# Kernel tuning notes

Measured on AMD Instinct MI355X. Metric: run time of the kernel, lower is better.

## Reference

```python
import math
import jax, jax.numpy as jnp
import numpy as np

B, T, E, H = 1, 2048, 2048, 16
D = E // H // 2  # head_dim = 64
DEPTH = 12
LAMBDA_INIT = 0.8 - 0.6 * math.exp(-0.3 * DEPTH)
EPS = 1e-5
NEG = -1e30


def rotary_cos_sin(seqlen, dim):
    # matches flash-attn RotaryEmbedding: inv_freq over even indices, base 10000
    inv_freq = 1.0 / (10000.0 ** (jnp.arange(0, dim, 2, dtype=jnp.float32) / dim))
    t = jnp.arange(seqlen, dtype=jnp.float32)
    freqs = jnp.outer(t, inv_freq)  # [T, D/2]
    return jnp.cos(freqs), jnp.sin(freqs)


def apply_rotary_interleaved(x, cos, sin):
    # x: [B, T, nH, D]; rotate interleaved pairs (x0,x1),(x2,x3),...
    x1 = x[..., 0::2]
    x2 = x[..., 1::2]
    c = cos[None, :, None, :]
    s = sin[None, :, None, :]
    o1 = x1 * c - x2 * s
    o2 = x1 * s + x2 * c
    return jnp.stack([o1, o2], axis=-1).reshape(x.shape)


def causal_attn_pair(q, k, v1, v2, mask, scale):
    # q,k,v*: [B, T, H, D]; shared softmax over (q,k), applied to both v1 and v2
    s = jnp.einsum('bthd,bshd->bhts', q, k) * scale
    s = jnp.where(mask, s, NEG)
    a = jax.nn.softmax(s, axis=-1)
    o1 = jnp.einsum('bhts,bshd->bthd', a, v1)
    o2 = jnp.einsum('bhts,bshd->bthd', a, v2)
    return jnp.concatenate([o1, o2], axis=-1)  # [B, T, H, 2D]


def setup_inputs() -> dict:
    key = jax.random.key(0)
    ks = jax.random.split(key, 10)
    return {
        'query': jax.random.normal(ks[0], (B, T, E), dtype=jnp.float32),
        'Wq': jax.random.normal(ks[1], (E, E), dtype=jnp.float32) * 0.02,
        'Wk': jax.random.normal(ks[2], (E, E), dtype=jnp.float32) * 0.02,
        'Wv': jax.random.normal(ks[3], (E, E), dtype=jnp.float32) * 0.02,
        'Wout': jax.random.normal(ks[4], (E, E), dtype=jnp.float32) * 0.02,
        'lambda_q1': jax.random.normal(ks[5], (D,), dtype=jnp.float32) * 0.1,
        'lambda_k1': jax.random.normal(ks[6], (D,), dtype=jnp.float32) * 0.1,
        'lambda_q2': jax.random.normal(ks[7], (D,), dtype=jnp.float32) * 0.1,
        'lambda_k2': jax.random.normal(ks[8], (D,), dtype=jnp.float32) * 0.1,
        'rms_weight': jnp.ones((2 * D,), dtype=jnp.float32),
    }


def reference(query, Wq, Wk, Wv, Wout, lambda_q1, lambda_k1, lambda_q2, lambda_k2, rms_weight):
    bsz, tgt_len, embed_dim = query.shape
    cos, sin = rotary_cos_sin(tgt_len, D)
    scale = D ** (-0.5)
    mask = jnp.tril(jnp.ones((tgt_len, tgt_len), dtype=bool))[None, None]

    q = (query @ Wq).reshape(bsz, tgt_len, 2 * H, D)
    k = (query @ Wk).reshape(bsz, tgt_len, 2 * H, D)
    v = (query @ Wv).reshape(bsz, tgt_len, H, 2, D)

    q = apply_rotary_emb = apply_rotary_interleaved(q, cos, sin)
    k = apply_rotary_interleaved(k, cos, sin)

    q = q.reshape(bsz, tgt_len, H, 2, D)
    k = k.reshape(bsz, tgt_len, H, 2, D)
    q1, q2 = q[:, :, :, 0], q[:, :, :, 1]
    k1, k2 = k[:, :, :, 0], k[:, :, :, 1]
    v1, v2 = v[:, :, :, 0], v[:, :, :, 1]

    attn1 = causal_attn_pair(q1, k1, v1, v2, mask, scale)  # [B,T,H,2D]
    attn2 = causal_attn_pair(q2, k2, v1, v2, mask, scale)

    lambda_1 = jnp.exp(jnp.sum(lambda_q1 * lambda_k1))
    lambda_2 = jnp.exp(jnp.sum(lambda_q2 * lambda_k2))
    lambda_full = lambda_1 - lambda_2 + LAMBDA_INIT

    f1 = jnp.fft.rfft(attn1, axis=1)
    f2 = jnp.fft.rfft(attn2, axis=1)
    attn_freq = f1 - lambda_full * f2

    n_freq = attn_freq.shape[1]
    sigma = 0.3 / 2.0  # cutoff_ratio / 2, gaussian window
    x = jnp.linspace(0.0, 1.0, n_freq)
    filt = jnp.exp(-0.5 * (x / sigma) ** 2)
    attn_freq = attn_freq * filt[None, :, None, None]

    attn = jnp.fft.irfft(attn_freq, n=tgt_len, axis=1)  # [B,T,H,2D]

    # RMSNorm over last dim (2*head_dim) with affine weight
    attn = attn * jax.lax.rsqrt(jnp.mean(attn * attn, axis=-1, keepdims=True) + EPS) * rms_weight
    attn = attn * (1.0 - LAMBDA_INIT)

    attn = attn.reshape(bsz, tgt_len, H * 2 * D)
    return attn @ Wout
```

## Files before the change

kernel.cpp:

```cpp
#include <hip/hip_runtime.h>
#include <math.h>

#define LAMBDA_INIT_F 0.7836057665316245f
#define ONE_MINUS_LI  0.2163942334683755f

typedef unsigned short ushort_t;
typedef unsigned int   uint32;
typedef unsigned long long u64;
typedef __attribute__((ext_vector_type(8))) short short8;
typedef __attribute__((ext_vector_type(4))) float f32x4;

__device__ __forceinline__ ushort_t f2bf(float f) {
    union { float f; uint32 u; } x; x.f = f;
    uint32 r = (x.u + 0x7fffu + ((x.u >> 16) & 1u)) >> 16;
    return (ushort_t)r;
}

__device__ __forceinline__ void gld16(ushort_t* lds, const ushort_t* g) {
    __builtin_amdgcn_global_load_lds(
        (const __attribute__((address_space(1))) uint32*)g,
        (__attribute__((address_space(3))) uint32*)lds,
        16, 0, 0);
}

__global__ __launch_bounds__(64) void lambda_kernel(
    const float* __restrict__ lq1, const float* __restrict__ lk1,
    const float* __restrict__ lq2, const float* __restrict__ lk2,
    float* __restrict__ lam)
{
    int l = threadIdx.x;
    float p1 = lq1[l] * lk1[l];
    float p2 = lq2[l] * lk2[l];
    for (int off = 32; off; off >>= 1) {
        p1 += __shfl_down(p1, off);
        p2 += __shfl_down(p2, off);
    }
    if (l == 0) lam[0] = expf(p1) - expf(p2) + LAMBDA_INIT_F;
}

__global__ __launch_bounds__(256) void gfilt_kernel(float* __restrict__ g)
{
    __shared__ float red[4];
    const int j = blockIdx.x;
    int tau = j - 64;
    int ta = tau < 0 ? -tau : tau;
    const int tid = threadIdx.x;
    float acc = 0.0f;
    for (int k = tid; k <= 1024; k += 256) {
        float w = (k == 0 || k == 1024) ? 1.0f : 2.0f;
        float r = (float)k * (1.0f / 153.6f);
        float f = expf(-0.5f * r * r);
        int m = (k * ta) & 2047;
        float ang = (float)m * 3.0679615757712823e-3f;
        acc += w * f * cosf(ang);
    }
    for (int off = 32; off; off >>= 1) acc += __shfl_down(acc, off);
    if ((tid & 63) == 0) red[tid >> 6] = acc;
    __syncthreads();
    if (tid == 0)
        g[j] = (red[0] + red[1] + red[2] + red[3]) * (1.0f / 2048.0f);
}

__global__ __launch_bounds__(256) void rottab(float* __restrict__ ct, float* __restrict__ st)
{
    int id = blockIdx.x * 256 + threadIdx.x;
    int t = id >> 5, i = id & 31;
    double inv = exp(-0.28782313662425575 * (double)i);
    double a = (double)t * inv;
    ct[id] = (float)cos(a);
    st[id] = (float)sin(a);
}

__global__ __launch_bounds__(256) void cvt_bf16(const float* __restrict__ s, ushort_t* __restrict__ d)
{
    int i = (blockIdx.x * 256 + threadIdx.x) * 8;
    float4 a = *(const float4*)(s + i);
    float4 b = *(const float4*)(s + i + 4);
    uint4 pk;
    pk.x = (uint32)f2bf(a.x) | ((uint32)f2bf(a.y) << 16);
    pk.y = (uint32)f2bf(a.z) | ((uint32)f2bf(a.w) << 16);
    pk.z = (uint32)f2bf(b.x) | ((uint32)f2bf(b.y) << 16);
    pk.w = (uint32)f2bf(b.z) | ((uint32)f2bf(b.w) << 16);
    *(uint4*)(d + i) = pk;
}

__global__ __launch_bounds__(256) void wtrans(
    const float* __restrict__ Wq, const float* __restrict__ Wk,
    const float* __restrict__ Wv, const float* __restrict__ Wo,
    ushort_t* __restrict__ Tq, ushort_t* __restrict__ Tk,
    ushort_t* __restrict__ Tv, ushort_t* __restrict__ To)
{
    int z = blockIdx.z;
    const float* S = (z == 0) ? Wq : (z == 1) ? Wk : (z == 2) ? Wv : Wo;
    ushort_t* Dt = (z == 0) ? Tq : (z == 1) ? Tk : (z == 2) ? Tv : To;
    bool perm = (z < 2);
    __shared__ float Ls[64 * 65];
    const int tid = threadIdx.x;
    const int n0 = blockIdx.x * 64, k0 = blockIdx.y * 64;
    #pragma unroll
    for (int it = 0; it < 4; ++it) {
        int kk = it * 16 + (tid >> 4);
        int nn = (tid & 15) * 4;
        float4 v = *(const float4*)(S + (size_t)(k0 + kk) * 2048 + n0 + nn);
        Ls[(nn + 0) * 65 + kk] = v.x;
        Ls[(nn + 1) * 65 + kk] = v.y;
        Ls[(nn + 2) * 65 + kk] = v.z;
        Ls[(nn + 3) * 65 + kk] = v.w;
    }
    __syncthreads();
    int nl = tid >> 2, kc = (tid & 3) * 16;
    int ng = n0 + nl;
    int nd = perm ? ((ng & ~63) | ((ng & 1) << 5) | ((ng & 63) >> 1)) : ng;
    uint4 p0, p1;
    const float* row = Ls + nl * 65 + kc;
    p0.x = (uint32)f2bf(row[0])  | ((uint32)f2bf(row[1])  << 16);
    p0.y = (uint32)f2bf(row[2])  | ((uint32)f2bf(row[3])  << 16);
    p0.z = (uint32)f2bf(row[4])  | ((uint32)f2bf(row[5])  << 16);
    p0.w = (uint32)f2bf(row[6])  | ((uint32)f2bf(row[7])  << 16);
    p1.x = (uint32)f2bf(row[8])  | ((uint32)f2bf(row[9])  << 16);
    p1.y = (uint32)f2bf(row[10]) | ((uint32)f2bf(row[11]) << 16);
    p1.z = (uint32)f2bf(row[12]) | ((uint32)f2bf(row[13]) << 16);
    p1.w = (uint32)f2bf(row[14]) | ((uint32)f2bf(row[15]) << 16);
    *(uint4*)(Dt + (size_t)nd * 2048 + k0 + kc) = p0;
    *(uint4*)(Dt + (size_t)nd * 2048 + k0 + kc + 8) = p1;
}

template<int QA, int QB, bool RA>
__device__ __forceinline__ void qkv_phase(
    const ushort_t* __restrict__ Ah, const ushort_t* __restrict__ Bh,
    short8 af[8], f32x4 acc[8][4], int wr, int wc, int quad, int l15)
{
    if (RA) {
        #pragma unroll
        for (int m = 0; m < 4; ++m)
            #pragma unroll
            for (int ks = 0; ks < 2; ++ks) {
                int r = wr * 64 + m * 16 + l15;
                af[m * 2 + ks] = *(const short8*)(Ah + r * 64 + ((ks * 4 + quad) ^ (r & 7)) * 8);
            }
    }
    short8 bfr[4];
    #pragma unroll
    for (int n = 0; n < 2; ++n)
        #pragma unroll
        for (int ks = 0; ks < 2; ++ks) {
            int r = (wc >> 1) * 64 + (wc & 1) * 16 + n * 32 + l15;
            bfr[n * 2 + ks] = *(const short8*)(Bh + r * 64 + ((ks * 4 + quad) ^ (r & 7)) * 8);
        }
    __builtin_amdgcn_s_setprio(1);
    #pragma unroll
    for (int m = 0; m < 4; ++m)
        #pragma unroll
        for (int n = 0; n < 2; ++n)
            #pragma unroll
            for (int ks = 0; ks < 2; ++ks)
                acc[QA * 4 + m][QB * 2 + n] = __builtin_amdgcn_mfma_f32_16x16x32_bf16(
                    af[m * 2 + ks], bfr[n * 2 + ks], acc[QA * 4 + m][QB * 2 + n], 0, 0, 0);
    __builtin_amdgcn_s_setprio(0);
}

#define PH_SYNC() do { __builtin_amdgcn_s_barrier(); __builtin_amdgcn_sched_barrier(0); } while (0)

__global__ __launch_bounds__(512, 2) void gemm_qkv(
    const ushort_t* __restrict__ A, const ushort_t* __restrict__ WT,
    ushort_t* __restrict__ q1, ushort_t* __restrict__ q2,
    ushort_t* __restrict__ k1, ushort_t* __restrict__ k2,
    ushort_t* __restrict__ v1T, ushort_t* __restrict__ v2T,
    const float* __restrict__ ctab, const float* __restrict__ stab)
{
    __shared__ ushort_t As[2][2][8192];
    __shared__ ushort_t Bs[2][2][8192];
    const int tid = threadIdx.x;
    const int w = tid >> 6, lane = tid & 63;
    const int quad = lane >> 4, l15 = lane & 15;
    const int wr = w >> 2, wc = w & 3;
    const int rb = blockIdx.y * 256, cbg = blockIdx.x * 256;

    auto stageA = [&](int pr, int ha, int tau) {
        int k0 = tau * 64;
        #pragma unroll
        for (int u = 0; u < 2; ++u) {
            int ci = w * 128 + u * 64 + lane;
            int row = ci >> 3, cc = (ci & 7) ^ (row & 7);
            gld16(&As[pr][ha][(w * 128 + u * 64) * 8],
                  A + (size_t)(rb + ha * 128 + row) * 2048 + k0 + cc * 8);
        }
    };
    auto stageB = [&](int pr, int hb, int tau) {
        int k0 = tau * 64;
        #pragma unroll
        for (int u = 0; u < 2; ++u) {
            int ci = w * 128 + u * 64 + lane;
            int row = ci >> 3, cc = (ci & 7) ^ (row & 7);
            gld16(&Bs[pr][hb][(w * 128 + u * 64) * 8],
                  WT + (size_t)(cbg + hb * 128 + row) * 2048 + k0 + cc * 8);
        }
    };

    stageA(0, 0, 0); stageB(0, 0, 0);
    stageA(0, 1, 0); stageB(0, 1, 0);
    stageA(1, 0, 1); stageB(1, 0, 1);

    f32x4 acc[8][4];
    #pragma unroll
    for (int i = 0; i < 8; ++i)
        #pragma unroll
        for (int j = 0; j < 4; ++j) acc[i][j] = (f32x4)0.0f;
    short8 af[8];

    for (int it = 0; it < 16; ++it) {
        const int t = it * 2;
        const int t2 = (t + 2 < 32) ? t + 2 : 31;
        const int t3 = (t + 3 < 32) ? t + 3 : 31;
        asm volatile("s_waitcnt vmcnt(8)" ::: "memory");
        PH_SYNC();
        stageA(1, 1, t + 1);
        qkv_phase<0, 0, true >(As[0][0], Bs[0][0], af, acc, wr, wc, quad, l15);
        asm volatile("s_waitcnt vmcnt(6)" ::: "memory");
        PH_SYNC();
        stageB(1, 1, t + 1);
        qkv_phase<0, 1, false>(As[0][0], Bs[0][1], af, acc, wr, wc, quad, l15);
        PH_SYNC();
        stageA(0, 0, t2);
        qkv_phase<1, 0, true >(As[0][1], Bs[0][0], af, acc, wr, wc, quad, l15);
        PH_SYNC();
        stageB(0, 0, t2);
        qkv_phase<1, 1, false>(As[0][1], Bs[0][1], af, acc, wr, wc, quad, l15);
        asm volatile("s_waitcnt vmcnt(8)" ::: "memory");
        PH_SYNC();
        stageA(0, 1, t2);
        qkv_phase<0, 0, true >(As[1][0], Bs[1][0], af, acc, wr, wc, quad, l15);
        asm volatile("s_waitcnt vmcnt(6)" ::: "memory");
        PH_SYNC();
        stageB(0, 1, t2);
        qkv_phase<0, 1, false>(As[1][0], Bs[1][1], af, acc, wr, wc, quad, l15);
        PH_SYNC();
        stageA(1, 0, t3);
        qkv_phase<1, 0, true >(As[1][1], Bs[1][0], af, acc, wr, wc, quad, l15);
        PH_SYNC();
        stageB(1, 0, t3);
        qkv_phase<1, 1, false>(As[1][1], Bs[1][1], af, acc, wr, wc, quad, l15);
    }

    const int region = cbg >> 11;
    const int nloc = cbg & 2047;
    if (region < 2) {
        ushort_t* b1 = region ? k1 : q1;
        ushort_t* b2 = region ? k2 : q2;
        const int i = (wc & 1) * 16 + l15;
        #pragma unroll
        for (int qb = 0; qb < 2; ++qb) {
            int head2 = (nloc >> 6) + qb * 2 + (wc >> 1);
            ushort_t* dst = ((head2 & 1) ? b2 : b1) + (size_t)(head2 >> 1) * 2048 * 64;
            #pragma unroll
            for (int mi = 0; mi < 8; ++mi)
                #pragma unroll
                for (int r = 0; r < 4; ++r) {
                    int t = rb + (mi >> 2) * 128 + wr * 64 + (mi & 3) * 16 + quad * 4 + r;
                    float c = ctab[t * 32 + i], s = stab[t * 32 + i];
                    float x1 = acc[mi][qb * 2 + 0][r], x2 = acc[mi][qb * 2 + 1][r];
                    dst[(size_t)t * 64 + i]      = f2bf(x1 * c - x2 * s);
                    dst[(size_t)t * 64 + 32 + i] = f2bf(x1 * s + x2 * c);
                }
        }
    } else {
        #pragma unroll
        for (int mi = 0; mi < 8; ++mi)
            #pragma unroll
            for (int nj = 0; nj < 4; ++nj) {
                int cg = nloc + (nj >> 1) * 128 + (wc >> 1) * 64 + (wc & 1) * 16
                       + (nj & 1) * 32 + l15;
                int hh = cg >> 7, pr = (cg >> 6) & 1, d = cg & 63;
                int tb = rb + (mi >> 2) * 128 + wr * 64 + (mi & 3) * 16 + quad * 4;
                ushort_t* dst = (pr ? v2T : v1T) + ((size_t)(hh * 64 + d)) * 2048 + tb;
                u64 pk = (u64)f2bf(acc[mi][nj][0])
                       | ((u64)f2bf(acc[mi][nj][1]) << 16)
                       | ((u64)f2bf(acc[mi][nj][2]) << 32)
                       | ((u64)f2bf(acc[mi][nj][3]) << 48);
                *(u64*)dst = pk;
            }
    }
}

#define PSTRIDE 88

__device__ __forceinline__ void attn_step(
    const ushort_t* __restrict__ Kb, const ushort_t* __restrict__ V1b,
    const ushort_t* __restrict__ V2b, ushort_t* __restrict__ pw,
    const short8* qb, f32x4* O, float& m_i, float& l_i,
    int quad, int l15, int row_l, bool diag)
{
    f32x4 s[4];
    #pragma unroll
    for (int j = 0; j < 4; ++j) s[j] = (f32x4)0.0f;
    #pragma unroll
    for (int ks = 0; ks < 2; ++ks)
        #pragma unroll
        for (int j = 0; j < 4; ++j) {
            int r = j * 16 + l15;
            short8 kf = *(const short8*)(Kb + r * 64 + ((ks * 4 + quad) ^ (r & 7)) * 8);
            s[j] = __builtin_amdgcn_mfma_f32_16x16x32_bf16(kf, qb[ks], s[j], 0, 0, 0);
        }
    float mx = -1e30f;
    #pragma unroll
    for (int j = 0; j < 4; ++j)
        #pragma unroll
        for (int r = 0; r < 4; ++r) {
            float v = s[j][r] * 0.125f;
            if (diag) {
                int kp = j * 16 + quad * 4 + r;
                v = (kp <= row_l) ? v : -1e30f;
            }
            s[j][r] = v;
            mx = fmaxf(mx, v);
        }
    mx = fmaxf(mx, __shfl_xor(mx, 16));
    mx = fmaxf(mx, __shfl_xor(mx, 32));
    float newm = fmaxf(m_i, mx);
    float alpha = __expf(m_i - newm);
    float sum = 0.0f;
    #pragma unroll
    for (int j = 0; j < 4; ++j) {
        float p0 = __expf(s[j][0] - newm);
        float p1 = __expf(s[j][1] - newm);
        float p2 = __expf(s[j][2] - newm);
        float p3 = __expf(s[j][3] - newm);
        sum += (p0 + p1) + (p2 + p3);
        u64 pk = (u64)f2bf(p0) | ((u64)f2bf(p1) << 16)
               | ((u64)f2bf(p2) << 32) | ((u64)f2bf(p3) << 48);
        *(u64*)(pw + l15 * PSTRIDE + j * 16 + quad * 4) = pk;
    }
    sum += __shfl_xor(sum, 16);
    sum += __shfl_xor(sum, 32);
    l_i = l_i * alpha + sum;
    m_i = newm;
    float av0 = __shfl(alpha, quad * 4 + 0);
    float av1 = __shfl(alpha, quad * 4 + 1);
    float av2 = __shfl(alpha, quad * 4 + 2);
    float av3 = __shfl(alpha, quad * 4 + 3);
    #pragma unroll
    for (int nt = 0; nt < 8; ++nt) {
        O[nt][0] *= av0; O[nt][1] *= av1; O[nt][2] *= av2; O[nt][3] *= av3;
    }
    #pragma unroll
    for (int ks = 0; ks < 2; ++ks) {
        short8 pf = *(const short8*)(pw + l15 * PSTRIDE + ks * 32 + quad * 8);
        #pragma unroll
        for (int nt = 0; nt < 8; ++nt) {
            const ushort_t* Vs = (nt < 4) ? V1b : V2b;
            int d = (nt & 3) * 16 + l15;
            short8 vf = *(const short8*)(Vs + d * 64 + ((ks * 4 + quad) ^ (d & 7)) * 8);
            O[nt] = __builtin_amdgcn_mfma_f32_16x16x32_bf16(pf, vf, O[nt], 0, 0, 0);
        }
    }
}

__global__ __launch_bounds__(512, 4) void attn_pipe(
    const ushort_t* __restrict__ q1, const ushort_t* __restrict__ k1,
    const ushort_t* __restrict__ q2, const ushort_t* __restrict__ k2,
    const ushort_t* __restrict__ v1T, const ushort_t* __restrict__ v2T,
    float* __restrict__ X, const float* __restrict__ lam_ptr)
{
    __shared__ ushort_t Tt[4][4096];
    __shared__ ushort_t Ps[8][16 * PSTRIDE];

    const int tid = threadIdx.x;
    const int w = tid >> 6, lane = tid & 63;
    const int quad = lane >> 4, l15 = lane & 15;
    const int pair = w >> 2, wl = w & 3;
    const int b = blockIdx.x;
    const int h = b & 15;
    const int x16 = (b & 255) >> 4;
    const int qt = (b < 256) ? (31 - x16) : x16;
    const float lam = lam_ptr[0];
    const int row_l = wl * 16 + l15;

    const ushort_t* k1h = k1 + (size_t)h * 2048 * 64;
    const ushort_t* k2h = k2 + (size_t)h * 2048 * 64;
    const ushort_t* v1h = v1T + (size_t)h * 64 * 2048;
    const ushort_t* v2h = v2T + (size_t)h * 64 * 2048;

    short8 qb[2];
    {
        const ushort_t* qp = (pair ? q2 : q1)
            + ((size_t)h * 2048 + qt * 64 + wl * 16 + l15) * 64 + quad * 8;
        qb[0] = *(const short8*)(qp);
        qb[1] = *(const short8*)(qp + 32);
    }

    const int ci = tid;
    const int srow = ci >> 3, scc = (ci & 7) ^ (srow & 7);
    const int koff = srow * 64 + scc * 8;
    const int voff = srow * 2048 + scc * 8;

    short8 sK1, sK2, sV1, sV2;

    sK1 = *(const short8*)(k1h + koff);
    sK2 = *(const short8*)(k2h + koff);
    sV1 = *(const short8*)(v1h + voff);
    sV2 = *(const short8*)(v2h + voff);
    *(short8*)(&Tt[0][ci * 8]) = sK1;
    *(short8*)(&Tt[1][ci * 8]) = sK2;
    *(short8*)(&Tt[2][ci * 8]) = sV1;
    *(short8*)(&Tt[3][ci * 8]) = sV2;
    __syncthreads();

    f32x4 O[8];
    #pragma unroll
    for (int i = 0; i < 8; ++i) O[i] = (f32x4)0.0f;
    float m_i = -1e30f, l_i = 0.0f;

    const ushort_t* Kb = Tt[pair];

    for (int kt = 0; kt <= qt; ++kt) {
        if (kt < qt) {
            int kb = (kt + 1) * 4096, vb = (kt + 1) * 64;
            sK1 = *(const short8*)(k1h + kb + koff);
            sK2 = *(const short8*)(k2h + kb + koff);
            sV1 = *(const short8*)(v1h + vb + voff);
            sV2 = *(const short8*)(v2h + vb + voff);
        }
        attn_step(Kb, Tt[2], Tt[3], &Ps[w][0], qb, O, m_i, l_i,
                  quad, l15, row_l, kt == qt);
        __syncthreads();
        if (kt < qt) {
            *(short8*)(&Tt[0][ci * 8]) = sK1;
            *(short8*)(&Tt[1][ci * 8]) = sK2;
            *(short8*)(&Tt[2][ci * 8]) = sV1;
            *(short8*)(&Tt[3][ci * 8]) = sV2;
            __syncthreads();
        }
    }

    float sc = pair ? lam : 1.0f;
    float rr0 = sc / __shfl(l_i, quad * 4 + 0);
    float rr1 = sc / __shfl(l_i, quad * 4 + 1);
    float rr2 = sc / __shfl(l_i, quad * 4 + 2);
    float rr3 = sc / __shfl(l_i, quad * 4 + 3);

    float* LX = (float*)&Tt[0][0];
    const int rbase = wl * 16 + quad * 4;
    if (pair) {
        #pragma unroll
        for (int nt = 0; nt < 8; ++nt) {
            int cb = nt * 16 + l15;
            LX[(rbase + 0) * 128 + cb] = O[nt][0] * rr0;
            LX[(rbase + 1) * 128 + cb] = O[nt][1] * rr1;
            LX[(rbase + 2) * 128 + cb] = O[nt][2] * rr2;
            LX[(rbase + 3) * 128 + cb] = O[nt][3] * rr3;
        }
    }
    __syncthreads();
    if (!pair) {
        int tb = qt * 64 + rbase;
        #pragma unroll
        for (int nt = 0; nt < 8; ++nt) {
            int cb = nt * 16 + l15;
            int col = h * 128 + cb;
            X[(size_t)(tb + 0) * 2048 + col] = O[nt][0] * rr0 - LX[(rbase + 0) * 128 + cb];
            X[(size_t)(tb + 1) * 2048 + col] = O[nt][1] * rr1 - LX[(rbase + 1) * 128 + cb];
            X[(size_t)(tb + 2) * 2048 + col] = O[nt][2] * rr2 - LX[(rbase + 2) * 128 + cb];
            X[(size_t)(tb + 3) * 2048 + col] = O[nt][3] * rr3 - LX[(rbase + 3) * 128 + cb];
        }
    }
}

__global__ __launch_bounds__(256) void conv_t(
    const float* __restrict__ X, const float* __restrict__ g, float* __restrict__ Y)
{
    __shared__ float Xs[192 * 64];
    __shared__ float gs[129];
    const int tid = threadIdx.x;
    const int c0 = blockIdx.x * 64, t0 = blockIdx.y * 64;
    const int c = tid & 63, tg = tid >> 6;
    for (int j = tg; j < 192; j += 4)
        Xs[j * 64 + c] = X[(size_t)((t0 - 64 + j) & 2047) * 2048 + c0 + c];
    if (tid < 129) gs[tid] = g[tid];
    __syncthreads();
    float accv[16];
    #pragma unroll
    for (int i = 0; i < 16; ++i) accv[i] = 0.0f;
    const int tl0 = tg * 16;
    for (int tap = 0; tap < 129; ++tap) {
        float gv = gs[tap];
        int base = (tl0 + 128 - tap) * 64 + c;
        #pragma unroll
        for (int i = 0; i < 16; ++i) accv[i] += gv * Xs[base + i * 64];
    }
    #pragma unroll
    for (int i = 0; i < 16; ++i)
        Y[(size_t)(t0 + tl0 + i) * 2048 + c0 + c] = accv[i];
}

__global__ __launch_bounds__(64) void rms_bf(
    const float* __restrict__ Y, const float* __restrict__ wgt, ushort_t* __restrict__ yb)
{
    int grp = blockIdx.x;
    int t = grp >> 4, hh = grp & 15, l = threadIdx.x;
    size_t base = (size_t)t * 2048 + hh * 128;
    float a = Y[base + l];
    float b = Y[base + 64 + l];
    float ss = a * a + b * b;
    for (int off = 32; off; off >>= 1) ss += __shfl_down(ss, off);
    ss = __shfl(ss, 0);
    float r = rsqrtf(ss * (1.0f / 128.0f) + 1e-5f) * ONE_MINUS_LI;
    yb[base + l]      = f2bf(a * r * wgt[l]);
    yb[base + 64 + l] = f2bf(b * r * wgt[64 + l]);
}

__global__ __launch_bounds__(256) void gemm_out(
    const ushort_t* __restrict__ A, const ushort_t* __restrict__ BT,
    float* __restrict__ C)
{
    __shared__ ushort_t As[4096];
    __shared__ ushort_t Bs[8192];
    const int tid = threadIdx.x;
    const int w = tid >> 6, lane = tid & 63;
    const int quad = lane >> 4, l15 = lane & 15;
    const int wr = w >> 1, wc = w & 1;
    const int rb = blockIdx.y * 64, cb = blockIdx.x * 128;

    f32x4 acc[2][4];
    #pragma unroll
    for (int i = 0; i < 2; ++i)
        #pragma unroll
        for (int j = 0; j < 4; ++j) acc[i][j] = (f32x4)0.0f;

    for (int k0 = 0; k0 < 2048; k0 += 64) {
        #pragma unroll
        for (int u = 0; u < 2; ++u) {
            int off = (w * 2 + u) * 512;
            int Lc = (off >> 3) + lane;
            int row = Lc >> 3, cc = (Lc & 7) ^ (row & 7);
            gld16(As + off, A + (size_t)(rb + row) * 2048 + k0 + cc * 8);
        }
        #pragma unroll
        for (int u = 0; u < 4; ++u) {
            int off = (w * 4 + u) * 512;
            int Lc = (off >> 3) + lane;
            int row = Lc >> 3, cc = (Lc & 7) ^ (row & 7);
            gld16(Bs + off, BT + (size_t)(cb + row) * 2048 + k0 + cc * 8);
        }
        __syncthreads();
        #pragma unroll
        for (int ks = 0; ks < 2; ++ks) {
            short8 af[2], bfr[4];
            #pragma unroll
            for (int mi = 0; mi < 2; ++mi) {
                int r = wr * 32 + mi * 16 + l15;
                af[mi] = *(const short8*)(As + r * 64 + ((ks * 4 + quad) ^ (r & 7)) * 8);
            }
            #pragma unroll
            for (int nj = 0; nj < 4; ++nj) {
                int r = wc * 64 + nj * 16 + l15;
                bfr[nj] = *(const short8*)(Bs + r * 64 + ((ks * 4 + quad) ^ (r & 7)) * 8);
            }
            #pragma unroll
            for (int mi = 0; mi < 2; ++mi)
                #pragma unroll
                for (int nj = 0; nj < 4; ++nj)
                    acc[mi][nj] = __builtin_amdgcn_mfma_f32_16x16x32_bf16(
                        af[mi], bfr[nj], acc[mi][nj], 0, 0, 0);
        }
        __syncthreads();
    }

    #pragma unroll
    for (int mi = 0; mi < 2; ++mi)
        #pragma unroll
        for (int nj = 0; nj < 4; ++nj) {
            int cg = cb + wc * 64 + nj * 16 + l15;
            #pragma unroll
            for (int r = 0; r < 4; ++r) {
                int t = rb + wr * 32 + mi * 16 + quad * 4 + r;
                C[(size_t)t * 2048 + cg] = acc[mi][nj][r];
            }
        }
}

extern "C" void kernel_launch(void* const* d_in, const int* in_sizes, int n_in,
                              void* d_out, int out_size, void* d_ws, size_t ws_size,
                              hipStream_t stream)
{
    const float* query = (const float*)d_in[0];
    const float* Wq    = (const float*)d_in[1];
    const float* Wk    = (const float*)d_in[2];
    const float* Wv    = (const float*)d_in[3];
    const float* Wout  = (const float*)d_in[4];
    const float* lq1   = (const float*)d_in[5];
    const float* lk1   = (const float*)d_in[6];
    const float* lq2   = (const float*)d_in[7];
    const float* lk2   = (const float*)d_in[8];
    const float* rmsw  = (const float*)d_in[9];
    float* out = (float*)d_out;

    const size_t MB = 1ull << 20;
    char* W = (char*)d_ws;
    ushort_t* WqT   = (ushort_t*)(W + 0 * MB);
    ushort_t* WkT   = (ushort_t*)(W + 8 * MB);
    ushort_t* WvT   = (ushort_t*)(W + 16 * MB);
    ushort_t* WoutT = (ushort_t*)(W + 24 * MB);
    ushort_t* qb    = (ushort_t*)(W + 32 * MB);
    ushort_t* q1    = (ushort_t*)(W + 40 * MB);
    ushort_t* q2    = (ushort_t*)(W + 44 * MB);
    ushort_t* k1    = (ushort_t*)(W + 48 * MB);
    ushort_t* k2    = (ushort_t*)(W + 52 * MB);
    ushort_t* v1T   = (ushort_t*)(W + 56 * MB);
    ushort_t* v2T   = (ushort_t*)(W + 60 * MB);
    float*    X     = (float*)   (W + 64 * MB);
    float*    Y     = (float*)   (W + 32 * MB);
    ushort_t* ybf   = (ushort_t*)(W + 48 * MB);
    float*    ctab  = (float*)   (W + 80 * MB);
    float*    stab  = (float*)   (W + 80 * MB + 256 * 1024);
    float*    gbuf  = (float*)   (W + 80 * MB + 512 * 1024);
    float*    lam   = (float*)   (W + 80 * MB + 520 * 1024);

    lambda_kernel<<<1, 64, 0, stream>>>(lq1, lk1, lq2, lk2, lam);
    gfilt_kernel<<<129, 256, 0, stream>>>(gbuf);
    rottab<<<256, 256, 0, stream>>>(ctab, stab);
    cvt_bf16<<<2048, 256, 0, stream>>>(query, qb);
    wtrans<<<dim3(32, 32, 4), 256, 0, stream>>>(Wq, Wk, Wv, Wout, WqT, WkT, WvT, WoutT);

    gemm_qkv<<<dim3(24, 8), 512, 0, stream>>>(qb, WqT, q1, q2, k1, k2, v1T, v2T, ctab, stab);

    attn_pipe<<<512, 512, 0, stream>>>(q1, k1, q2, k2, v1T, v2T, X, lam);

    conv_t<<<dim3(32, 32), 256, 0, stream>>>(X, gbuf, Y);
    rms_bf<<<32768, 64, 0, stream>>>(Y, rmsw, ybf);

    gemm_out<<<dim3(16, 32), 256, 0, stream>>>(ybf, WoutT, out);
}
```

Measured before the change: 337.8 us.

## Restructure QKV GEMM main loop into ping-pong phases with explicit LDS waits

The QKV projection GEMM loop is rescheduled so each phase issues its LDS fragment reads and the next global-to-LDS prefetch first, then synchronizes with barriers and an explicit lgkmcnt(0) wait before the MFMA block. The vmcnt waits are moved and the staging order changes, with separate named LDS buffers in place of the indexed array. The aim is to overlap LDS reads and global prefetch with MFMA work across waves and to give the scheduler clearer phase boundaries. The added barriers per phase and the changed prefetch order could add sync overhead or expose races if the wait counts are off.

```diff
diff --git a/kernel.cpp b/kernel.cpp
--- a/kernel.cpp
+++ b/kernel.cpp
@@ -125,28 +125,33 @@
     *(uint4*)(Dt + (size_t)nd * 2048 + k0 + kc + 8) = p1;
 }
 
-template<int QA, int QB, bool RA>
-__device__ __forceinline__ void qkv_phase(
-    const ushort_t* __restrict__ Ah, const ushort_t* __restrict__ Bh,
-    short8 af[8], f32x4 acc[8][4], int wr, int wc, int quad, int l15)
-{
-    if (RA) {
-        #pragma unroll
-        for (int m = 0; m < 4; ++m)
-            #pragma unroll
-            for (int ks = 0; ks < 2; ++ks) {
-                int r = wr * 64 + m * 16 + l15;
-                af[m * 2 + ks] = *(const short8*)(Ah + r * 64 + ((ks * 4 + quad) ^ (r & 7)) * 8);
-            }
-    }
-    short8 bfr[4];
-    #pragma unroll
-    for (int n = 0; n < 2; ++n)
-        #pragma unroll
-        for (int ks = 0; ks < 2; ++ks) {
-            int r = (wc >> 1) * 64 + (wc & 1) * 16 + n * 32 + l15;
-            bfr[n * 2 + ks] = *(const short8*)(Bh + r * 64 + ((ks * 4 + quad) ^ (r & 7)) * 8);
-        }
+#define SB()    __builtin_amdgcn_s_barrier()
+#define LGKM0() asm volatile("s_waitcnt lgkmcnt(0)" ::: "memory")
+#define VM6()   asm volatile("s_waitcnt vmcnt(6)" ::: "memory")
+
+__device__ __forceinline__ void rdA(short8 af[8], const ushort_t* Ah, int rbase, int quad)
+{
+    #pragma unroll
+    for (int m = 0; m < 4; ++m) {
+        int r = rbase + m * 16;
+        #pragma unroll
+        for (int ks = 0; ks < 2; ++ks)
+            af[m * 2 + ks] = *(const short8*)(Ah + r * 64 + ((ks * 4 + quad) ^ (r & 7)) * 8);
+    }
+}
+__device__ __forceinline__ void rdB(short8 bf[4], const ushort_t* Bh, int rbase, int quad)
+{
+    #pragma unroll
+    for (int n = 0; n < 2; ++n) {
+        int r = rbase + n * 32;
+        #pragma unroll
+        for (int ks = 0; ks < 2; ++ks)
+            bf[n * 2 + ks] = *(const short8*)(Bh + r * 64 + ((ks * 4 + quad) ^ (r & 7)) * 8);
+    }
+}
+template<int QA, int QB>
+__device__ __forceinline__ void mfma16(const short8 af[8], const short8 bf[4], f32x4 acc[8][4])
+{
     __builtin_amdgcn_s_setprio(1);
     #pragma unroll
     for (int m = 0; m < 4; ++m)
@@ -155,11 +160,9 @@
             #pragma unroll
             for (int ks = 0; ks < 2; ++ks)
                 acc[QA * 4 + m][QB * 2 + n] = __builtin_amdgcn_mfma_f32_16x16x32_bf16(
-                    af[m * 2 + ks], bfr[n * 2 + ks], acc[QA * 4 + m][QB * 2 + n], 0, 0, 0);
+                    af[m * 2 + ks], bf[n * 2 + ks], acc[QA * 4 + m][QB * 2 + n], 0, 0, 0);
     __builtin_amdgcn_s_setprio(0);
 }
-
-#define PH_SYNC() do { __builtin_amdgcn_s_barrier(); __builtin_amdgcn_sched_barrier(0); } while (0)
 
 __global__ __launch_bounds__(512, 2) void gemm_qkv(
     const ushort_t* __restrict__ A, const ushort_t* __restrict__ WT,
@@ -168,78 +171,78 @@
     ushort_t* __restrict__ v1T, ushort_t* __restrict__ v2T,
     const float* __restrict__ ctab, const float* __restrict__ stab)
 {
-    __shared__ ushort_t As[2][2][8192];
-    __shared__ ushort_t Bs[2][2][8192];
+    __shared__ ushort_t sA0h0[8192], sA0h1[8192], sA1h0[8192], sA1h1[8192];
+    __shared__ ushort_t sB0h0[8192], sB0h1[8192], sB1h0[8192], sB1h1[8192];
     const int tid = threadIdx.x;
     const int w = tid >> 6, lane = tid & 63;
     const int quad = lane >> 4, l15 = lane & 15;
     const int wr = w >> 2, wc = w & 3;
     const int rb = blockIdx.y * 256, cbg = blockIdx.x * 256;
-
-    auto stageA = [&](int pr, int ha, int tau) {
-        int k0 = tau * 64;
+    const int rA = wr * 64 + l15;
+    const int rB = (wc >> 1) * 64 + (wc & 1) * 16 + l15;
+    const int cib = w * 128;
+
+    auto stA = [&](ushort_t* buf, int ha, int tau) {
         #pragma unroll
         for (int u = 0; u < 2; ++u) {
-            int ci = w * 128 + u * 64 + lane;
+            int ci = cib + u * 64 + lane;
             int row = ci >> 3, cc = (ci & 7) ^ (row & 7);
-            gld16(&As[pr][ha][(w * 128 + u * 64) * 8],
-                  A + (size_t)(rb + ha * 128 + row) * 2048 + k0 + cc * 8);
+            gld16(buf + (cib + u * 64) * 8,
+                  A + (size_t)(rb + ha * 128 + row) * 2048 + tau * 64 + cc * 8);
         }
     };
-    auto stageB = [&](int pr, int hb, int tau) {
-        int k0 = tau * 64;
+    auto stB = [&](ushort_t* buf, int hb, int tau) {
         #pragma unroll
         for (int u = 0; u < 2; ++u) {
-            int ci = w * 128 + u * 64 + lane;
+            int ci = cib + u * 64 + lane;
             int row = ci >> 3, cc = (ci & 7) ^ (row & 7);
-            gld16(&Bs[pr][hb][(w * 128 + u * 64) * 8],
-                  WT + (size_t)(cbg + hb * 128 + row) * 2048 + k0 + cc * 8);
+            gld16(buf + (cib + u * 64) * 8,
+                  WT + (size_t)(cbg + hb * 128 + row) * 2048 + tau * 64 + cc * 8);
         }
     };
 
-    stageA(0, 0, 0); stageB(0, 0, 0);
-    stageA(0, 1, 0); stageB(0, 1, 0);
-    stageA(1, 0, 1); stageB(1, 0, 1);
+    stA(sA0h0, 0, 0); stA(sA0h1, 1, 0); stB(sB0h0, 0, 0); stB(sB0h1, 1, 0);
+    stA(sA1h0, 0, 1); stA(sA1h1, 1, 1); stB(sB1h0, 0, 1);
 
     f32x4 acc[8][4];
     #pragma unroll
     for (int i = 0; i < 8; ++i)
         #pragma unroll
         for (int j = 0; j < 4; ++j) acc[i][j] = (f32x4)0.0f;
-    short8 af[8];
+    short8 af[8], bf[4];
+
+    VM6();
+    SB();
 
     for (int it = 0; it < 16; ++it) {
         const int t = it * 2;
+        const int t1 = t + 1;
         const int t2 = (t + 2 < 32) ? t + 2 : 31;
         const int t3 = (t + 3 < 32) ? t + 3 : 31;
-        asm volatile("s_waitcnt vmcnt(8)" ::: "memory");
-        PH_SYNC();
-        stageA(1, 1, t + 1);
-        qkv_phase<0, 0, true >(As[0][0], Bs[0][0], af, acc, wr, wc, quad, l15);
-        asm volatile("s_waitcnt vmcnt(6)" ::: "memory");
-        PH_SYNC();
-        stageB(1, 1, t + 1);
-        qkv_phase<0, 1, false>(As[0][0], Bs[0][1], af, acc, wr, wc, quad, l15);
-        PH_SYNC();
-        stageA(0, 0, t2);
-        qkv_phase<1, 0, true >(As[0][1], Bs[0][0], af, acc, wr, wc, quad, l15);
-        PH_SYNC();
-        stageB(0, 0, t2);
-        qkv_phase<1, 1, false>(As[0][1], Bs[0][1], af, acc, wr, wc, quad, l15);
-        asm volatile("s_waitcnt vmcnt(8)" ::: "memory");
-        PH_SYNC();
-        stageA(0, 1, t2);
-        qkv_phase<0, 0, true >(As[1][0], Bs[1][0], af, acc, wr, wc, quad, l15);
-        asm volatile("s_waitcnt vmcnt(6)" ::: "memory");
-        PH_SYNC();
-        stageB(0, 1, t2);
-        qkv_phase<0, 1, false>(As[1][0], Bs[1][1], af, acc, wr, wc, quad, l15);
-        PH_SYNC();
-        stageA(1, 0, t3);
-        qkv_phase<1, 0, true >(As[1][1], Bs[1][0], af, acc, wr, wc, quad, l15);
-        PH_SYNC();
-        stageB(1, 0, t3);
-        qkv_phase<1, 1, false>(As[1][1], Bs[1][1], af, acc, wr, wc, quad, l15);
+        rdA(af, sA0h0, rA, quad); rdB(bf, sB0h0, rB, quad);
+        stB(sB1h1, 1, t1);
+        SB(); LGKM0(); mfma16<0, 0>(af, bf, acc); SB();
+        rdB(bf, sB0h1, rB, quad);
+        stA(sA0h0, 0, t2);
+        SB(); LGKM0(); mfma16<0, 1>(af, bf, acc); SB();
+        rdA(af, sA0h1, rA, quad); rdB(bf, sB0h0, rB, quad);
+        SB(); LGKM0(); mfma16<1, 0>(af, bf, acc); SB();
+        rdB(bf, sB0h1, rB, quad);
+        stA(sA0h1, 1, t2); stB(sB0h0, 0, t2);
+        VM6();
+        SB(); LGKM0(); mfma16<1, 1>(af, bf, acc); SB();
+        rdA(af, sA1h0, rA, quad); rdB(bf, sB1h0, rB, quad);
+        stB(sB0h1, 1, t2);
+        SB(); LGKM0(); mfma16<0, 0>(af, bf, acc); SB();
+        rdB(bf, sB1h1, rB, quad);
+        stA(sA1h0, 0, t3);
+        SB(); LGKM0(); mfma16<0, 1>(af, bf, acc); SB();
+        rdA(af, sA1h1, rA, quad); rdB(bf, sB1h0, rB, quad);
+        SB(); LGKM0(); mfma16<1, 0>(af, bf, acc); SB();
+        rdB(bf, sB1h1, rB, quad);
+        stA(sA1h1, 1, t3); stB(sB1h0, 0, t3);
+        VM6();
+        SB(); LGKM0(); mfma16<1, 1>(af, bf, acc); SB();
     }
 
     const int region = cbg >> 11;
```

After: 326.7 us. 1.03x faster.
